# Optimization experiments

Measured on AMD Instinct MI355X. Metric: run time of the kernel, lower is better.

## Reference

```python
import jax, jax.numpy as jnp
import numpy as np

B, F = 1024, 784
OUT, OR_T, AND_T = 1024, 32, 16
IDX_RANGE = 1 + 2 * F  # column 0 is the constant-true column


def setup_inputs() -> dict:
    key = jax.random.key(0)
    kx, kw = jax.random.split(key)
    # Binary inputs (0/1) stored as float32; module calls x.bool() i.e. x != 0.
    x = jax.random.randint(kx, (B, F), 0, 2).astype(jnp.float32)
    # Integer gate wiring: indices into [const_true | x | ~x].
    weights = jax.random.randint(kw, (OUT, OR_T, AND_T), 0, IDX_RANGE).astype(jnp.int32)
    return {"x": x, "weights": weights}


def reference(x, weights):
    out_f, or_t, and_t = weights.shape
    b = x.shape[0]
    xb = x != 0                                            # [B, F] bool
    ones = jnp.ones((b, 1), dtype=bool)
    x_in = jnp.concatenate([ones, xb, ~xb], axis=1)        # [B, 1+2F]
    # or_padding_mask: an OR-term is active unless all its AND indices are 0
    or_mask = ~jnp.all(weights == 0, axis=-1)              # [OUT, OR_T]
    # Gather selected booleans, then AND over and_terms, OR over or_terms
    x_sel = x_in[:, weights.reshape(-1)]                   # [B, OUT*OR_T*AND_T]
    x_bin = x_sel.reshape(b, out_f, or_t, and_t)
    x_and = jnp.all(x_bin, axis=-1) & or_mask              # [B, OUT, OR_T]
    x_or = jnp.any(x_and, axis=-1)                         # [B, OUT]
    return x_or
```

## Files before the change

kernel.cpp:

```cpp
#include <hip/hip_runtime.h>
#include <stdint.h>

#define BATCH 1024
#define FEAT  784
#define OUTF  1024
#define OR_T  32
#define AND_T 16
#define NIDX  1569
#define BSTRIDE 1600
#define NGROUP  16

typedef unsigned long long u64;

__global__ __launch_bounds__(64) void pack_bits(const float* __restrict__ x,
                                                u64* __restrict__ bits) {
    const int g    = blockIdx.x;
    const int fb   = blockIdx.y;
    const int lane = threadIdx.x;
    const float4* xrow = (const float4*)(x + (size_t)(g * 64 + lane) * FEAT);
    u64* bg = bits + (size_t)g * BSTRIDE;

    for (int i = 0; i < 28; ++i) {
        const int f4 = fb * 28 + i;
        const float4 v = xrow[f4];
        const int f = f4 * 4;
        const u64 m0 = __ballot(v.x != 0.0f);
        const u64 m1 = __ballot(v.y != 0.0f);
        const u64 m2 = __ballot(v.z != 0.0f);
        const u64 m3 = __ballot(v.w != 0.0f);
        const u64 mv = (lane == 0) ? m0 : (lane == 1) ? m1 : (lane == 2) ? m2 : m3;
        if (lane < 4) {
            bg[1 + f + lane]   = mv;
            bg[785 + f + lane] = ~mv;
        }
    }
    if (fb == 0 && lane == 0) bg[0] = ~0ull;
}

__global__ __launch_bounds__(1024) void eval_logic(const int* __restrict__ w,
                                                   const u64* __restrict__ bits,
                                                   int* __restrict__ out) {
    __shared__ u64 lbits[BSTRIDE];
    __shared__ u64 red[1024];

    const int g   = blockIdx.x;
    const int ob  = blockIdx.y;
    const int tid = threadIdx.x;

    const u64* bg = bits + (size_t)g * BSTRIDE;
    for (int i = tid; i < BSTRIDE; i += 1024) lbits[i] = bg[i];
    __syncthreads();

    const int o_local = tid & 63;
    const int tg      = tid >> 6;
    const int o       = ob * 64 + o_local;

    const int4* wq = (const int4*)(w + ((size_t)o * OR_T + tg * 2) * AND_T);

    u64 orv = 0;
    #pragma unroll
    for (int tt = 0; tt < 2; ++tt) {
        u64 a = ~0ull;
        int zor = 0;
        #pragma unroll
        for (int k = 0; k < 4; ++k) {
            const int4 wi = wq[tt * 4 + k];
            zor |= wi.x | wi.y | wi.z | wi.w;
            a &= lbits[wi.x];
            a &= lbits[wi.y];
            a &= lbits[wi.z];
            a &= lbits[wi.w];
        }
        if (zor != 0) orv |= a;
    }

    red[tid] = orv;
    __syncthreads();

    u64 full = 0;
    #pragma unroll
    for (int j = 0; j < 16; ++j) full |= red[o_local + j * 64];

    int* outg = out + (size_t)(g * 64) * OUTF + (size_t)ob * 64;
    #pragma unroll
    for (int jj = 0; jj < 4; ++jj) {
        const int j = tg * 4 + jj;
        outg[(size_t)j * OUTF + o_local] = (int)((full >> j) & 1);
    }
}

__global__ __launch_bounds__(1024) void binlayer_fused(const float* __restrict__ x,
                                                       const int* __restrict__ w,
                                                       int* __restrict__ out) {
    __shared__ u64 lbits[BSTRIDE];
    __shared__ u64 red[1024];

    const int g    = blockIdx.x;
    const int ob   = blockIdx.y;
    const int tid  = threadIdx.x;
    const int lane = tid & 63;
    const int wv   = tid >> 6;

    const int start = wv * 12 + (wv < 4 ? wv : 4);
    const int cnt   = (wv < 4) ? 13 : 12;
    const float4* xrow = (const float4*)(x + (size_t)(g * 64 + lane) * FEAT);
    for (int i = 0; i < cnt; ++i) {
        const int f4 = start + i;
        const float4 v = xrow[f4];
        const int f = f4 * 4;
        const u64 m0 = __ballot(v.x != 0.0f);
        const u64 m1 = __ballot(v.y != 0.0f);
        const u64 m2 = __ballot(v.z != 0.0f);
        const u64 m3 = __ballot(v.w != 0.0f);
        const u64 mv = (lane == 0) ? m0 : (lane == 1) ? m1 : (lane == 2) ? m2 : m3;
        if (lane < 4) {
            lbits[1 + f + lane]   = mv;
            lbits[785 + f + lane] = ~mv;
        }
    }
    if (tid == 0) lbits[0] = ~0ull;
    __syncthreads();

    const int o_local = tid & 63;
    const int tg      = tid >> 6;
    const int o       = ob * 64 + o_local;
    const int4* wq = (const int4*)(w + ((size_t)o * OR_T + tg * 2) * AND_T);

    u64 orv = 0;
    #pragma unroll
    for (int tt = 0; tt < 2; ++tt) {
        u64 a = ~0ull;
        int zor = 0;
        #pragma unroll
        for (int k = 0; k < 4; ++k) {
            const int4 wi = wq[tt * 4 + k];
            zor |= wi.x | wi.y | wi.z | wi.w;
            a &= lbits[wi.x];
            a &= lbits[wi.y];
            a &= lbits[wi.z];
            a &= lbits[wi.w];
        }
        if (zor != 0) orv |= a;
    }

    red[tid] = orv;
    __syncthreads();

    u64 full = 0;
    #pragma unroll
    for (int j = 0; j < 16; ++j) full |= red[o_local + j * 64];

    int* outg = out + (size_t)(g * 64) * OUTF + (size_t)ob * 64;
    #pragma unroll
    for (int jj = 0; jj < 4; ++jj) {
        const int j = tg * 4 + jj;
        outg[(size_t)j * OUTF + o_local] = (int)((full >> j) & 1);
    }
}

extern "C" void kernel_launch(void* const* d_in, const int* in_sizes, int n_in,
                              void* d_out, int out_size, void* d_ws, size_t ws_size,
                              hipStream_t stream) {
    const float* x = (const float*)d_in[0];
    const int*   w = (const int*)d_in[1];
    int* out = (int*)d_out;

    const size_t need = (size_t)NGROUP * BSTRIDE * sizeof(u64);
    if (ws_size >= need) {
        u64* bits = (u64*)d_ws;
        pack_bits<<<dim3(NGROUP, 7), 64, 0, stream>>>(x, bits);
        eval_logic<<<dim3(NGROUP, OUTF / 64), 1024, 0, stream>>>(w, bits, out);
    } else {
        binlayer_fused<<<dim3(NGROUP, OUTF / 64), 1024, 0, stream>>>(x, w, out);
    }
}
```

Measured before the change: 71.88 us.

## Transpose weights to output-major layout in a merged prep kernel for coalesced gathers

```diff
diff --git a/kernel.cpp b/kernel.cpp
--- a/kernel.cpp
+++ b/kernel.cpp
@@ -9,35 +9,81 @@
 #define NIDX  1569
 #define BSTRIDE 1600
 #define NGROUP  16
+#define TKDIM   512
+
+#define BITS_BYTES (NGROUP * BSTRIDE * 8)
+#define WT_OFF     208896
+#define WS_NEED    (WT_OFF + (size_t)TKDIM * OUTF * 4)
+
+#define NB_PACK 448
+#define NB_TR   128
 
 typedef unsigned long long u64;
 
-__global__ __launch_bounds__(64) void pack_bits(const float* __restrict__ x,
-                                                u64* __restrict__ bits) {
-    const int g    = blockIdx.x;
-    const int fb   = blockIdx.y;
-    const int lane = threadIdx.x;
-    const float4* xrow = (const float4*)(x + (size_t)(g * 64 + lane) * FEAT);
-    u64* bg = bits + (size_t)g * BSTRIDE;
-
-    for (int i = 0; i < 28; ++i) {
-        const int f4 = fb * 28 + i;
-        const float4 v = xrow[f4];
-        const int f = f4 * 4;
-        const u64 m0 = __ballot(v.x != 0.0f);
-        const u64 m1 = __ballot(v.y != 0.0f);
-        const u64 m2 = __ballot(v.z != 0.0f);
-        const u64 m3 = __ballot(v.w != 0.0f);
-        const u64 mv = (lane == 0) ? m0 : (lane == 1) ? m1 : (lane == 2) ? m2 : m3;
-        if (lane < 4) {
-            bg[1 + f + lane]   = mv;
-            bg[785 + f + lane] = ~mv;
-        }
-    }
-    if (fb == 0 && lane == 0) bg[0] = ~0ull;
-}
-
-__global__ __launch_bounds__(1024) void eval_logic(const int* __restrict__ w,
+__global__ __launch_bounds__(64) void prep(const float* __restrict__ x,
+                                           const int* __restrict__ w,
+                                           u64* __restrict__ bits,
+                                           int* __restrict__ wt) {
+    __shared__ int t2[64 * 65];
+    const int b   = blockIdx.x;
+    const int tid = threadIdx.x;
+
+    if (b < NB_PACK) {
+        const int g  = b / 28;
+        const int fb = b % 28;
+        const float4* xrow = (const float4*)(x + (size_t)(g * 64 + tid) * FEAT);
+        u64* bg = bits + (size_t)g * BSTRIDE;
+
+        #pragma unroll
+        for (int i = 0; i < 7; ++i) {
+            const int f4 = fb * 7 + i;
+            const float4 v = xrow[f4];
+            const int f = f4 * 4;
+            const u64 m0 = __ballot(v.x != 0.0f);
+            const u64 m1 = __ballot(v.y != 0.0f);
+            const u64 m2 = __ballot(v.z != 0.0f);
+            const u64 m3 = __ballot(v.w != 0.0f);
+            const u64 mv = (tid == 0) ? m0 : (tid == 1) ? m1 : (tid == 2) ? m2 : m3;
+            if (tid < 4) {
+                bg[1 + f + tid]   = mv;
+                bg[785 + f + tid] = ~mv;
+            }
+        }
+        if (fb == 0 && tid == 0) bg[0] = ~0ull;
+    } else {
+        const int b2     = b - NB_PACK;
+        const int o_base  = (b2 & 15) * 64;
+        const int tk_base = (b2 >> 4) * 64;
+
+        #pragma unroll
+        for (int i = 0; i < 16; ++i) {
+            const int idx = i * 64 + tid;
+            const int r = idx >> 4;
+            const int q = idx & 15;
+            const int4 v = *(const int4*)(w + (size_t)(o_base + r) * TKDIM
+                                            + tk_base + q * 4);
+            t2[(q * 4 + 0) * 65 + r] = v.x;
+            t2[(q * 4 + 1) * 65 + r] = v.y;
+            t2[(q * 4 + 2) * 65 + r] = v.z;
+            t2[(q * 4 + 3) * 65 + r] = v.w;
+        }
+        __syncthreads();
+        #pragma unroll
+        for (int i = 0; i < 16; ++i) {
+            const int idx = i * 64 + tid;
+            const int rr = idx >> 4;
+            const int qq = idx & 15;
+            int4 o4;
+            o4.x = t2[rr * 65 + qq * 4 + 0];
+            o4.y = t2[rr * 65 + qq * 4 + 1];
+            o4.z = t2[rr * 65 + qq * 4 + 2];
+            o4.w = t2[rr * 65 + qq * 4 + 3];
+            *(int4*)(wt + (size_t)(tk_base + rr) * OUTF + o_base + qq * 4) = o4;
+        }
+    }
+}
+
+__global__ __launch_bounds__(1024) void eval_logic(const int* __restrict__ wt,
                                                    const u64* __restrict__ bits,
                                                    int* __restrict__ out) {
     __shared__ u64 lbits[BSTRIDE];
@@ -55,21 +101,18 @@
     const int tg      = tid >> 6;
     const int o       = ob * 64 + o_local;
 
-    const int4* wq = (const int4*)(w + ((size_t)o * OR_T + tg * 2) * AND_T);
-
     u64 orv = 0;
     #pragma unroll
     for (int tt = 0; tt < 2; ++tt) {
+        const int term = tg * 2 + tt;
+        const int* wcol = wt + (size_t)(term * AND_T) * OUTF + o;
         u64 a = ~0ull;
         int zor = 0;
         #pragma unroll
-        for (int k = 0; k < 4; ++k) {
-            const int4 wi = wq[tt * 4 + k];
-            zor |= wi.x | wi.y | wi.z | wi.w;
-            a &= lbits[wi.x];
-            a &= lbits[wi.y];
-            a &= lbits[wi.z];
-            a &= lbits[wi.w];
+        for (int k = 0; k < 16; ++k) {
+            const int idx = wcol[(size_t)k * OUTF];
+            zor |= idx;
+            a &= lbits[idx];
         }
         if (zor != 0) orv |= a;
     }
@@ -165,11 +208,11 @@
     const int*   w = (const int*)d_in[1];
     int* out = (int*)d_out;
 
-    const size_t need = (size_t)NGROUP * BSTRIDE * sizeof(u64);
-    if (ws_size >= need) {
+    if (ws_size >= WS_NEED) {
         u64* bits = (u64*)d_ws;
-        pack_bits<<<dim3(NGROUP, 7), 64, 0, stream>>>(x, bits);
-        eval_logic<<<dim3(NGROUP, OUTF / 64), 1024, 0, stream>>>(w, bits, out);
+        int* wt   = (int*)((char*)d_ws + WT_OFF);
+        prep<<<NB_PACK + NB_TR, 64, 0, stream>>>(x, w, bits, wt);
+        eval_logic<<<dim3(NGROUP, OUTF / 64), 1024, 0, stream>>>(wt, bits, out);
     } else {
         binlayer_fused<<<dim3(NGROUP, OUTF / 64), 1024, 0, stream>>>(x, w, out);
     }
```

New measurement: 66.13 us. -8.0%, faster.
